# Kernel tuning notes

Hardware: AMD Instinct MI355X
Metric: run time of the kernel (lower is better)

## Reference

```python
import jax, jax.numpy as jnp
import numpy as np

LN_EPS = 1e-5


def setup_inputs() -> dict:
    key = jax.random.key(0)
    ks = jax.random.split(key, 6)
    b, s, din = 8, 8192, 448
    h, d = 8, 56  # num_heads, head_dim (state_dim // num_heads)
    eye = jnp.eye(d, dtype=jnp.float32)
    A = eye[None] * 0.1 + 0.01 * jax.random.normal(ks[0], (h, d, d), jnp.float32)
    B = jnp.eye(d, din, dtype=jnp.float32)[None] * 0.1 + 0.01 * jax.random.normal(ks[1], (h, d, din), jnp.float32)
    C = eye[None] * 0.1 + 0.01 * jax.random.normal(ks[2], (h, d, d), jnp.float32)
    x = jax.random.normal(ks[3], (b, s, din), jnp.float32)
    W = 0.02 * jax.random.normal(ks[4], (din, din), jnp.float32)
    return {
        "x": x,
        "A": A,
        "B": B,
        "C": C,
        "gamma": jnp.ones((din,), jnp.float32),
        "beta": jnp.zeros((din,), jnp.float32),
        "W": W,
        "bias": jnp.zeros((din,), jnp.float32),
    }


def reference(x, A, B, C, gamma, beta, W, bias):
    # x: [b, s, din]; A: [h, d, d]; B: [h, d, din]; C: [h, d, d]
    b, s, _ = x.shape
    h, d = A.shape[0], A.shape[1]
    # semiseparable structured mask over the state dim (lower-triangular)
    M = jnp.tril(jnp.ones((d, d), x.dtype))
    # h_block = x @ B^T  (per head); blocks are independent so vectorize over full seq
    hb = jnp.einsum('bsi,hdi->bhsd', x, B)
    # intermediate = h_block @ A
    z = jnp.einsum('bhsd,hde->bhse', hb, A)
    # apply structured (semiseparable) mask: z @ M
    zm = jnp.einsum('bhsd,de->bhse', z, M)
    # y_block = masked @ C^T
    y = jnp.einsum('bhsd,hod->bhso', zm, C)  # [b, h, s, d]
    # Faithful to torch: raw row-major reshape (b,h,s,d) -> (b,s,h*d)
    y = y.reshape(b, s, h * d)
    # LayerNorm over last dim
    mu = jnp.mean(y, axis=-1, keepdims=True)
    var = jnp.mean(jnp.square(y - mu), axis=-1, keepdims=True)
    yn = (y - mu) * jax.lax.rsqrt(var + LN_EPS) * gamma + beta
    # final linear (dropout = identity in eval mode)
    out = jnp.einsum('bsi,oi->bso', yn, W) + bias
    return out
```

## Files before the change

kernel.cpp:

```cpp
#include <hip/hip_runtime.h>

typedef float f32x4 __attribute__((ext_vector_type(4)));
typedef __bf16 bf16x8 __attribute__((ext_vector_type(8)));
typedef unsigned short us8 __attribute__((ext_vector_type(8)));
typedef unsigned short us4 __attribute__((ext_vector_type(4)));

#define DIN 448
#define NH 8
#define HD 56
#define MT 64
#define BK 32
#define NTILES 28
#define LDA 40
#define LDC 456
#define S_LEN 8192

__device__ __forceinline__ unsigned short f2bf(float f) {
  union { float f; unsigned int u; } v; v.f = f;
  unsigned int r = v.u + 0x7fffu + ((v.u >> 16) & 1u);
  return (unsigned short)(r >> 16);
}
__device__ __forceinline__ float bf2f(unsigned short h) {
  union { unsigned int u; float f; } v; v.u = ((unsigned int)h) << 16;
  return v.f;
}

__global__ void precompute_D(const float* __restrict__ A, const float* __restrict__ C,
                             float* __restrict__ D)
{
  __shared__ float sA[HD * HD], sC[HD * HD], sSA[HD * HD];
  const int h = blockIdx.x, tid = threadIdx.x;
  for (int i = tid; i < HD * HD; i += 256) { sA[i] = A[h * HD * HD + i]; sC[i] = C[h * HD * HD + i]; }
  __syncthreads();
  for (int i = tid; i < HD * HD; i += 256) {
    int d = i / HD, e = i % HD;
    float s = 0.f;
    for (int k = e; k < HD; ++k) s += sA[d * HD + k];
    sSA[i] = s;
  }
  __syncthreads();
  for (int i = tid; i < HD * HD; i += 256) {
    int d = i / HD, o = i % HD;
    float s = 0.f;
    for (int e = 0; e < HD; ++e) s += sSA[d * HD + e] * sC[o * HD + e];
    D[h * HD * HD + i] = s;
  }
}

__global__ void precompute_GT(const float* __restrict__ B, const float* __restrict__ D,
                              const float* __restrict__ W,
                              unsigned short* __restrict__ GT, unsigned short* __restrict__ Wb)
{
  const int blk = blockIdx.x, tid = threadIdx.x;
  if (blk < 784) {
    const int g = blk * 256 + tid;
    const int col = g % DIN;
    const int ho  = g / DIN;
    const int h = ho / HD, o = ho % HD;
    const float* Bh = B + (long)h * HD * DIN + col;
    const float* Dh = D + h * HD * HD + o;
    float s = 0.f;
#pragma unroll
    for (int d = 0; d < HD; ++d) s += Bh[d * DIN] * Dh[d * HD];
    GT[(long)ho * DIN + col] = f2bf(s);
  } else {
    const int g = (blk - 784) * 256 + tid;
    const float4 v = *(const float4*)(W + (long)g * 4);
    us4 hv; hv[0] = f2bf(v.x); hv[1] = f2bf(v.y); hv[2] = f2bf(v.z); hv[3] = f2bf(v.w);
    *(us4*)(Wb + (long)g * 4) = hv;
  }
}

union LdsU {
  struct { unsigned short a[MT * LDA]; unsigned short b[DIN * LDA]; } s;
  unsigned short c[MT * LDC];
};

template<int STAGE>
__global__ __launch_bounds__(256, 2)
void gemm_stage(const void* __restrict__ Ag, const unsigned short* __restrict__ Bt,
                const float* __restrict__ gamma, const float* __restrict__ beta,
                const float* __restrict__ bias,
                unsigned short* __restrict__ yn, float* __restrict__ out)
{
  __shared__ LdsU lds;
  const int tid  = threadIdx.x;
  const int wave = tid >> 6;
  const int lane = tid & 63;
  const int quad = lane >> 4;
  const int l16  = lane & 15;
  const long row0 = (long)blockIdx.x * MT;

  f32x4 acc[NTILES];
#pragma unroll
  for (int i = 0; i < NTILES; ++i) acc[i] = f32x4{0.f, 0.f, 0.f, 0.f};

  for (int kt = 0; kt < DIN / BK; ++kt) {
    const int k0 = kt * BK;
    __syncthreads();
    if (STAGE == 1) {
      const float* X = (const float*)Ag;
#pragma unroll
      for (int j = 0; j < 2; ++j) {
        int idx = j * 256 + tid;
        int r = idx >> 3, c4 = idx & 7;
        const float4 v = *(const float4*)(X + (row0 + r) * DIN + k0 + c4 * 4);
        us4 hv; hv[0] = f2bf(v.x); hv[1] = f2bf(v.y); hv[2] = f2bf(v.z); hv[3] = f2bf(v.w);
        *(us4*)(&lds.s.a[r * LDA + c4 * 4]) = hv;
      }
    } else {
      const unsigned short* Y = (const unsigned short*)Ag;
      int r = tid >> 2, c8 = tid & 3;
      us8 v = *(const us8*)(Y + (row0 + r) * DIN + k0 + c8 * 8);
      *(us8*)(&lds.s.a[r * LDA + c8 * 8]) = v;
    }
#pragma unroll
    for (int j = 0; j < 7; ++j) {
      int idx = j * 256 + tid;
      int n = idx >> 2, c8 = idx & 3;
      us8 v = *(const us8*)(Bt + (long)n * DIN + k0 + c8 * 8);
      *(us8*)(&lds.s.b[n * LDA + c8 * 8]) = v;
    }
    __syncthreads();
    bf16x8 af = *(const bf16x8*)(&lds.s.a[(wave * 16 + l16) * LDA + quad * 8]);
#pragma unroll
    for (int nt = 0; nt < NTILES; ++nt) {
      bf16x8 bfr = *(const bf16x8*)(&lds.s.b[(nt * 16 + l16) * LDA + quad * 8]);
      acc[nt] = __builtin_amdgcn_mfma_f32_16x16x32_bf16(af, bfr, acc[nt], 0, 0, 0);
    }
  }

  if (STAGE == 2) {
    const int mbase = wave * 16 + quad * 4;
#pragma unroll
    for (int nt = 0; nt < NTILES; ++nt) {
      const int col = nt * 16 + l16;
      const float bs = bias[col];
#pragma unroll
      for (int rg = 0; rg < 4; ++rg)
        out[(row0 + mbase + rg) * DIN + col] = acc[nt][rg] + bs;
    }
  } else {
    __syncthreads();
#pragma unroll
    for (int nt = 0; nt < NTILES; ++nt) {
      const int col = nt * 16 + l16;
#pragma unroll
      for (int rg = 0; rg < 4; ++rg)
        lds.c[(wave * 16 + quad * 4 + rg) * LDC + col] = f2bf(acc[nt][rg]);
    }
    __syncthreads();
    const int row_id = tid >> 2, sub = tid & 3;
    const int g = row_id >> 3, hh = row_id & 7;
    float sum = 0.f, sq = 0.f;
#pragma unroll
    for (int jj = 0; jj < 2; ++jj) {
      const int r = sub * 2 + jj;
#pragma unroll
      for (int d = 0; d < HD; ++d) {
        float v = bf2f(lds.c[(g * 8 + r) * LDC + hh * HD + d]);
        sum += v; sq += v * v;
      }
    }
    sum += __shfl_xor(sum, 1); sq += __shfl_xor(sq, 1);
    sum += __shfl_xor(sum, 2); sq += __shfl_xor(sq, 2);
    const float mean = sum * (1.f / 448.f);
    const float var  = sq * (1.f / 448.f) - mean * mean;
    const float rstd = rsqrtf(var + 1e-5f);
    const long b_idx = row0 >> 13;
    const int  q0    = (int)((row0 & (S_LEN - 1)) >> 3);
    const long sn    = (long)hh * 1024 + q0 + g;
    unsigned short* dst = yn + ((b_idx << 13) + sn) * DIN;
#pragma unroll
    for (int jj = 0; jj < 2; ++jj) {
      const int r = sub * 2 + jj;
#pragma unroll
      for (int d = 0; d < HD; ++d) {
        const int f = r * HD + d;
        float v = bf2f(lds.c[(g * 8 + r) * LDC + hh * HD + d]);
        v = (v - mean) * rstd * gamma[f] + beta[f];
        dst[f] = f2bf(v);
      }
    }
  }
}

extern "C" void kernel_launch(void* const* d_in, const int* in_sizes, int n_in,
                              void* d_out, int out_size, void* d_ws, size_t ws_size,
                              hipStream_t stream)
{
  const float* x     = (const float*)d_in[0];
  const float* A     = (const float*)d_in[1];
  const float* B     = (const float*)d_in[2];
  const float* C     = (const float*)d_in[3];
  const float* gamma = (const float*)d_in[4];
  const float* beta  = (const float*)d_in[5];
  const float* W     = (const float*)d_in[6];
  const float* bias  = (const float*)d_in[7];
  float* out = (float*)d_out;

  char* ws = (char*)d_ws;
  unsigned short* GT = (unsigned short*)ws;
  unsigned short* Wb = (unsigned short*)(ws + 401408);
  unsigned short* yn = (unsigned short*)(ws + 802816);
  float* Dws = (float*)(ws + 802816);

  precompute_D<<<8, 256, 0, stream>>>(A, C, Dws);
  precompute_GT<<<980, 256, 0, stream>>>(B, Dws, W, GT, Wb);
  gemm_stage<1><<<1024, 256, 0, stream>>>(x, GT, gamma, beta, bias, yn, out);
  gemm_stage<2><<<1024, 256, 0, stream>>>(yn, Wb, gamma, beta, bias, yn, out);
}
```

Before: 365.3 us.

## Retile GEMMs to 128x224 with 512 threads and direct global-to-LDS loads

Both GEMM stages move from 64-row, full-width tiles (256 threads) to 128x224 tiles split over 8 waves arranged 4x2. Each wave now reuses its A and B fragments across 2x7 MFMAs instead of reloading B for every tile. bf16 operands are loaded with global_load_lds straight into unpadded LDS, and the LayerNorm epilogue uses vectorised 16-byte LDS reads and global stores. Each head now sits in one N-half, so the per-row reduction takes 8 lanes. Dropping the padding may cause LDS bank conflicts, and there is still no double buffering, so loads and MFMAs stay serialised.

```diff
diff --git a/kernel.cpp b/kernel.cpp
--- a/kernel.cpp
+++ b/kernel.cpp
@@ -6,13 +6,12 @@
 typedef unsigned short us4 __attribute__((ext_vector_type(4)));
 
 #define DIN 448
-#define NH 8
 #define HD 56
-#define MT 64
+#define MT 128
+#define NT 224
 #define BK 32
-#define NTILES 28
-#define LDA 40
-#define LDC 456
+#define KTI (DIN / BK)
+#define LDC 232
 #define S_LEN 8192
 
 __device__ __forceinline__ unsigned short f2bf(float f) {
@@ -23,6 +22,11 @@
 __device__ __forceinline__ float bf2f(unsigned short h) {
   union { unsigned int u; float f; } v; v.u = ((unsigned int)h) << 16;
   return v.f;
+}
+__device__ __forceinline__ void gload_lds16(const unsigned short* g, unsigned short* l) {
+  __builtin_amdgcn_global_load_lds(
+      (const __attribute__((address_space(1))) unsigned int*)g,
+      (__attribute__((address_space(3))) unsigned int*)l, 16, 0, 0);
 }
 
 __global__ void precompute_D(const float* __restrict__ A, const float* __restrict__ C,
@@ -71,116 +75,136 @@
   }
 }
 
-union LdsU {
-  struct { unsigned short a[MT * LDA]; unsigned short b[DIN * LDA]; } s;
-  unsigned short c[MT * LDC];
-};
-
 template<int STAGE>
-__global__ __launch_bounds__(256, 2)
+__global__ __launch_bounds__(512, 4)
 void gemm_stage(const void* __restrict__ Ag, const unsigned short* __restrict__ Bt,
                 const float* __restrict__ gamma, const float* __restrict__ beta,
                 const float* __restrict__ bias,
                 unsigned short* __restrict__ yn, float* __restrict__ out)
 {
-  __shared__ LdsU lds;
+  __shared__ union {
+    struct { unsigned short a[MT * BK]; unsigned short b[NT * BK]; } s;
+    unsigned short c[MT * LDC];
+  } lds;
   const int tid  = threadIdx.x;
   const int wave = tid >> 6;
   const int lane = tid & 63;
   const int quad = lane >> 4;
   const int l16  = lane & 15;
-  const long row0 = (long)blockIdx.x * MT;
-
-  f32x4 acc[NTILES];
-#pragma unroll
-  for (int i = 0; i < NTILES; ++i) acc[i] = f32x4{0.f, 0.f, 0.f, 0.f};
-
-  for (int kt = 0; kt < DIN / BK; ++kt) {
+  const int wm   = wave >> 1;
+  const int wn   = wave & 1;
+  const int  ntile = blockIdx.x & 1;
+  const long mtile = blockIdx.x >> 1;
+  const long row0  = mtile * MT;
+  const int  nc0   = ntile * NT;
+
+  const int gl_r = lane >> 2;
+  const int gl_k = (lane & 3) * 8;
+  const unsigned short* Bt_n = Bt + (long)nc0 * DIN;
+
+  f32x4 acc[2][7];
+#pragma unroll
+  for (int i = 0; i < 2; ++i)
+#pragma unroll
+    for (int j = 0; j < 7; ++j) acc[i][j] = f32x4{0.f, 0.f, 0.f, 0.f};
+
+  for (int kt = 0; kt < KTI; ++kt) {
     const int k0 = kt * BK;
-    __syncthreads();
     if (STAGE == 1) {
       const float* X = (const float*)Ag;
-#pragma unroll
-      for (int j = 0; j < 2; ++j) {
-        int idx = j * 256 + tid;
-        int r = idx >> 3, c4 = idx & 7;
-        const float4 v = *(const float4*)(X + (row0 + r) * DIN + k0 + c4 * 4);
-        us4 hv; hv[0] = f2bf(v.x); hv[1] = f2bf(v.y); hv[2] = f2bf(v.z); hv[3] = f2bf(v.w);
-        *(us4*)(&lds.s.a[r * LDA + c4 * 4]) = hv;
-      }
+      const int r = tid >> 2, q = (tid & 3) * 8;
+      const float* p = X + (row0 + r) * DIN + k0 + q;
+      const float4 v0 = *(const float4*)(p);
+      const float4 v1 = *(const float4*)(p + 4);
+      us8 hv;
+      hv[0] = f2bf(v0.x); hv[1] = f2bf(v0.y); hv[2] = f2bf(v0.z); hv[3] = f2bf(v0.w);
+      hv[4] = f2bf(v1.x); hv[5] = f2bf(v1.y); hv[6] = f2bf(v1.z); hv[7] = f2bf(v1.w);
+      *(us8*)(&lds.s.a[r * BK + q]) = hv;
     } else {
       const unsigned short* Y = (const unsigned short*)Ag;
-      int r = tid >> 2, c8 = tid & 3;
-      us8 v = *(const us8*)(Y + (row0 + r) * DIN + k0 + c8 * 8);
-      *(us8*)(&lds.s.a[r * LDA + c8 * 8]) = v;
-    }
+      gload_lds16(Y + (row0 + wave * 16 + gl_r) * DIN + k0 + gl_k,
+                  &lds.s.a[wave * 512]);
+    }
+    gload_lds16(Bt_n + (long)(wave * 16 + gl_r) * DIN + k0 + gl_k,
+                &lds.s.b[wave * 512]);
+    if (wave < 6)
+      gload_lds16(Bt_n + (long)(128 + wave * 16 + gl_r) * DIN + k0 + gl_k,
+                  &lds.s.b[4096 + wave * 512]);
+    __syncthreads();
+    {
+      const bf16x8 af0 = *(const bf16x8*)(&lds.s.a[(wm * 32 + l16) * BK + quad * 8]);
+      const bf16x8 af1 = *(const bf16x8*)(&lds.s.a[(wm * 32 + 16 + l16) * BK + quad * 8]);
+#pragma unroll
+      for (int j = 0; j < 7; ++j) {
+        const bf16x8 bfr = *(const bf16x8*)(&lds.s.b[(wn * 112 + j * 16 + l16) * BK + quad * 8]);
+        acc[0][j] = __builtin_amdgcn_mfma_f32_16x16x32_bf16(af0, bfr, acc[0][j], 0, 0, 0);
+        acc[1][j] = __builtin_amdgcn_mfma_f32_16x16x32_bf16(af1, bfr, acc[1][j], 0, 0, 0);
+      }
+    }
+    __syncthreads();
+  }
+
+  if (STAGE == 2) {
 #pragma unroll
     for (int j = 0; j < 7; ++j) {
-      int idx = j * 256 + tid;
-      int n = idx >> 2, c8 = idx & 3;
-      us8 v = *(const us8*)(Bt + (long)n * DIN + k0 + c8 * 8);
-      *(us8*)(&lds.s.b[n * LDA + c8 * 8]) = v;
-    }
+      const int col = nc0 + wn * 112 + j * 16 + l16;
+      const float bs = bias[col];
+#pragma unroll
+      for (int i = 0; i < 2; ++i)
+#pragma unroll
+        for (int rg = 0; rg < 4; ++rg)
+          out[(row0 + wm * 32 + i * 16 + quad * 4 + rg) * DIN + col] = acc[i][j][rg] + bs;
+    }
+  } else {
+#pragma unroll
+    for (int i = 0; i < 2; ++i)
+#pragma unroll
+      for (int j = 0; j < 7; ++j) {
+        const int col  = wn * 112 + j * 16 + l16;
+        const int rowb = wm * 32 + i * 16 + quad * 4;
+#pragma unroll
+        for (int rg = 0; rg < 4; ++rg)
+          lds.c[(rowb + rg) * LDC + col] = f2bf(acc[i][j][rg]);
+      }
     __syncthreads();
-    bf16x8 af = *(const bf16x8*)(&lds.s.a[(wave * 16 + l16) * LDA + quad * 8]);
-#pragma unroll
-    for (int nt = 0; nt < NTILES; ++nt) {
-      bf16x8 bfr = *(const bf16x8*)(&lds.s.b[(nt * 16 + l16) * LDA + quad * 8]);
-      acc[nt] = __builtin_amdgcn_mfma_f32_16x16x32_bf16(af, bfr, acc[nt], 0, 0, 0);
-    }
-  }
-
-  if (STAGE == 2) {
-    const int mbase = wave * 16 + quad * 4;
-#pragma unroll
-    for (int nt = 0; nt < NTILES; ++nt) {
-      const int col = nt * 16 + l16;
-      const float bs = bias[col];
-#pragma unroll
-      for (int rg = 0; rg < 4; ++rg)
-        out[(row0 + mbase + rg) * DIN + col] = acc[nt][rg] + bs;
-    }
-  } else {
-    __syncthreads();
-#pragma unroll
-    for (int nt = 0; nt < NTILES; ++nt) {
-      const int col = nt * 16 + l16;
-#pragma unroll
-      for (int rg = 0; rg < 4; ++rg)
-        lds.c[(wave * 16 + quad * 4 + rg) * LDC + col] = f2bf(acc[nt][rg]);
-    }
-    __syncthreads();
-    const int row_id = tid >> 2, sub = tid & 3;
-    const int g = row_id >> 3, hh = row_id & 7;
+    const int row_id = tid >> 3, sub = tid & 7;
+    const int g = row_id >> 2, hl = row_id & 3;
+    const unsigned short* src = &lds.c[(g * 8 + sub) * LDC + hl * HD];
     float sum = 0.f, sq = 0.f;
 #pragma unroll
-    for (int jj = 0; jj < 2; ++jj) {
-      const int r = sub * 2 + jj;
-#pragma unroll
-      for (int d = 0; d < HD; ++d) {
-        float v = bf2f(lds.c[(g * 8 + r) * LDC + hh * HD + d]);
-        sum += v; sq += v * v;
-      }
+    for (int c = 0; c < 7; ++c) {
+      const us8 u = *(const us8*)(src + c * 8);
+#pragma unroll
+      for (int e = 0; e < 8; ++e) { const float f = bf2f(u[e]); sum += f; sq += f * f; }
     }
     sum += __shfl_xor(sum, 1); sq += __shfl_xor(sq, 1);
     sum += __shfl_xor(sum, 2); sq += __shfl_xor(sq, 2);
+    sum += __shfl_xor(sum, 4); sq += __shfl_xor(sq, 4);
     const float mean = sum * (1.f / 448.f);
-    const float var  = sq * (1.f / 448.f) - mean * mean;
-    const float rstd = rsqrtf(var + 1e-5f);
+    const float rstd = rsqrtf(sq * (1.f / 448.f) - mean * mean + 1e-5f);
+    const int  hh    = ntile * 4 + hl;
+    const long q0    = (row0 & (S_LEN - 1)) >> 3;
     const long b_idx = row0 >> 13;
-    const int  q0    = (int)((row0 & (S_LEN - 1)) >> 3);
-    const long sn    = (long)hh * 1024 + q0 + g;
-    unsigned short* dst = yn + ((b_idx << 13) + sn) * DIN;
-#pragma unroll
-    for (int jj = 0; jj < 2; ++jj) {
-      const int r = sub * 2 + jj;
-#pragma unroll
-      for (int d = 0; d < HD; ++d) {
-        const int f = r * HD + d;
-        float v = bf2f(lds.c[(g * 8 + r) * LDC + hh * HD + d]);
-        v = (v - mean) * rstd * gamma[f] + beta[f];
-        dst[f] = f2bf(v);
-      }
+    unsigned short* dst = yn + ((b_idx << 13) + (long)hh * 1024 + q0 + g) * DIN + sub * HD;
+    const float* gp = gamma + sub * HD;
+    const float* bp = beta  + sub * HD;
+#pragma unroll
+    for (int c = 0; c < 7; ++c) {
+      const us8 u = *(const us8*)(src + c * 8);
+      const float4 g0 = *(const float4*)(gp + c * 8);
+      const float4 g1 = *(const float4*)(gp + c * 8 + 4);
+      const float4 b0 = *(const float4*)(bp + c * 8);
+      const float4 b1 = *(const float4*)(bp + c * 8 + 4);
+      us8 o;
+      o[0] = f2bf((bf2f(u[0]) - mean) * rstd * g0.x + b0.x);
+      o[1] = f2bf((bf2f(u[1]) - mean) * rstd * g0.y + b0.y);
+      o[2] = f2bf((bf2f(u[2]) - mean) * rstd * g0.z + b0.z);
+      o[3] = f2bf((bf2f(u[3]) - mean) * rstd * g0.w + b0.w);
+      o[4] = f2bf((bf2f(u[4]) - mean) * rstd * g1.x + b1.x);
+      o[5] = f2bf((bf2f(u[5]) - mean) * rstd * g1.y + b1.y);
+      o[6] = f2bf((bf2f(u[6]) - mean) * rstd * g1.z + b1.z);
+      o[7] = f2bf((bf2f(u[7]) - mean) * rstd * g1.w + b1.w);
+      *(us8*)(dst + c * 8) = o;
     }
   }
 }
@@ -207,6 +231,6 @@
 
   precompute_D<<<8, 256, 0, stream>>>(A, C, Dws);
   precompute_GT<<<980, 256, 0, stream>>>(B, Dws, W, GT, Wb);
-  gemm_stage<1><<<1024, 256, 0, stream>>>(x, GT, gamma, beta, bias, yn, out);
-  gemm_stage<2><<<1024, 256, 0, stream>>>(yn, Wb, gamma, beta, bias, yn, out);
-}
+  gemm_stage<1><<<1024, 512, 0, stream>>>(x, GT, gamma, beta, bias, yn, out);
+  gemm_stage<2><<<1024, 512, 0, stream>>>(yn, Wb, gamma, beta, bias, yn, out);
+}
```

After: 345.1 us. -5.5%, faster.
